# Kernel tuning notes

Hardware: AMD Instinct MI355X
Metric: run time of the kernel (lower is better)

The kernel has to match this reference:

```python
import jax, jax.numpy as jnp
import numpy as np

B, H, W, K = 4, 512, 512, 8
BKG_DEPTH = 100.0  # sentinel depth for empty pixels, as in the torch module


def setup_inputs() -> dict:
    key = jax.random.key(0)
    k1, k2, k3 = jax.random.split(key, 3)
    pixel_colors = jax.random.uniform(k1, (B, H, W, K, 4), dtype=jnp.float32)
    zbuf = jax.random.normal(k2, (B, H, W, K), dtype=jnp.float32)  # <0 => invalid fragment
    pixel_labels = jax.random.randint(k3, (B, H, W, K), 0, K, dtype=jnp.int32)
    background_color = jnp.ones((3,), jnp.float32)
    return {
        "pixel_colors": pixel_colors,
        "zbuf": zbuf,
        "pixel_labels": pixel_labels,
        "background_color": background_color,
    }


def _composite(pixel_colors, zbuf, labels_f, background_color):
    """Back-to-front alpha-over compositing scan across the K layer axis."""
    Bq, Hq, Wq, Kd, _ = pixel_colors.shape
    # layer axis to front, reversed so scan runs k = K-1 .. 0 (back to front)
    cols = jnp.moveaxis(pixel_colors, 3, 0)[::-1]  # [K,B,H,W,4]
    deps = jnp.moveaxis(zbuf, 3, 0)[::-1]          # [K,B,H,W]
    labs = jnp.moveaxis(labels_f, 3, 0)[::-1]      # [K,B,H,W]

    rgb0 = jnp.broadcast_to(background_color.astype(pixel_colors.dtype), (Bq, Hq, Wq, 3)) + 0.0
    a0 = jnp.zeros((Bq, Hq, Wq), pixel_colors.dtype)
    d0 = jnp.full((Bq, Hq, Wq), BKG_DEPTH, pixel_colors.dtype)
    l0 = jnp.full((Bq, Hq, Wq), float(Kd), pixel_colors.dtype)

    def step(carry, x):
        rgb, a, d, lab = carry
        c, z, l = x
        alpha = c[..., 3]
        rgb = c[..., :3] * alpha[..., None] + rgb * (1.0 - alpha[..., None])
        a = jnp.maximum(alpha, a)
        d = jnp.where(z > 0, z * alpha + d * (1.0 - alpha), d)
        lab = jnp.where(jnp.isfinite(l), jnp.where(alpha > 0.5, l, lab), lab)
        return (rgb, a, d, lab), None

    (rgb, a, d, lab), _ = jax.lax.scan(step, (rgb0, a0, d0, l0), (cols, deps, labs))
    img = jnp.concatenate([rgb, a[..., None]], axis=-1)  # [B,H,W,4]
    return img, d, lab


def _human_images(pixel_colors, labels_int, background_color):
    """For each label n in [0,K): gather the first (front-most) fragment with that label."""
    Bq, Hq, Wq, Kd, C = pixel_colors.shape
    N = Kd
    hit = labels_int[..., None] == jnp.arange(N, dtype=labels_int.dtype)  # [B,H,W,K,N]
    hit = jnp.concatenate([hit, jnp.ones((Bq, Hq, Wq, 1, N), bool)], axis=3)  # void layer always hits
    first = jnp.argmax(hit, axis=3)  # [B,H,W,N], first k where label matches, else K
    pcv = jnp.concatenate(
        [pixel_colors, jnp.zeros((Bq, Hq, Wq, 1, C), pixel_colors.dtype)], axis=3
    )  # [B,H,W,K+1,4]
    gathered = jnp.take_along_axis(pcv, first[..., None], axis=3)  # [B,H,W,N,4]
    alpha = gathered[..., 3:4]
    rgb = gathered[..., :3] * alpha + background_color * (1.0 - alpha)
    return jnp.concatenate([rgb, alpha], axis=-1)  # [B,H,W,N,4]


def reference(pixel_colors, zbuf, pixel_labels, background_color):
    Kd = pixel_colors.shape[3]
    # labels as float with NaN marking invalid fragments (zbuf < 0), as in torch forward
    labels_f = jnp.where(zbuf < 0, jnp.nan, pixel_labels.astype(pixel_colors.dtype))
    composite_image, composite_depth, lab = _composite(pixel_colors, zbuf, labels_f, background_color)
    # labels as ints with -1 marking invalid, as in raster_each_labeled_human
    labels_int = jnp.where(zbuf < 0, -1, pixel_labels.astype(jnp.int32))
    human_images = _human_images(pixel_colors, labels_int, background_color)
    lab = jnp.where(lab > Kd - 0.5, -1.0, lab)
    composite_label = jnp.round(lab).astype(jnp.int32)
    return composite_image, composite_depth, composite_label, human_images
```

## Files before the change

kernel.cpp:

```cpp
#include <hip/hip_runtime.h>


#define BKG_DEPTH 100.0f
#define KD 8

__global__ __launch_bounds__(256) void alpha_comp_kernel(
    const float4* __restrict__ pc,
    const float4* __restrict__ zb,
    const int4*  __restrict__ lb,
    const float* __restrict__ bg,
    float* __restrict__ out,
    int P)
{
    int pix = blockIdx.x * blockDim.x + threadIdx.x;
    if (pix >= P) return;

    const float bg0 = bg[0], bg1 = bg[1], bg2 = bg[2];

    float4 c[KD];
#pragma unroll
    for (int k = 0; k < KD; ++k) c[k] = pc[(size_t)pix * KD + k];

    float4 z0 = zb[(size_t)pix * 2 + 0];
    float4 z1 = zb[(size_t)pix * 2 + 1];
    float z[KD] = {z0.x, z0.y, z0.z, z0.w, z1.x, z1.y, z1.z, z1.w};

    int4 l0 = lb[(size_t)pix * 2 + 0];
    int4 l1 = lb[(size_t)pix * 2 + 1];
    int lbl[KD] = {l0.x, l0.y, l0.z, l0.w, l1.x, l1.y, l1.z, l1.w};

    float r = bg0, g = bg1, b = bg2;
    float a = 0.0f, d = BKG_DEPTH, lab = (float)KD;
#pragma unroll
    for (int k = KD - 1; k >= 0; --k) {
        const float alpha = c[k].w;
        const float ia = 1.0f - alpha;
        r = c[k].x * alpha + r * ia;
        g = c[k].y * alpha + g * ia;
        b = c[k].z * alpha + b * ia;
        a = fmaxf(alpha, a);
        if (z[k] > 0.0f) d = z[k] * alpha + d * ia;
        if (!(z[k] < 0.0f) && alpha > 0.5f) lab = (float)lbl[k];
    }
    const float labv = (lab > (float)KD - 0.5f) ? -1.0f : lab;

    float4 hv[KD];
#pragma unroll
    for (int n = 0; n < KD; ++n) {
        float4 gat = make_float4(0.0f, 0.0f, 0.0f, 0.0f);
#pragma unroll
        for (int k = KD - 1; k >= 0; --k) {
            if (!(z[k] < 0.0f) && lbl[k] == n) gat = c[k];
        }
        const float alpha = gat.w;
        const float ia = 1.0f - alpha;
        hv[n] = make_float4(gat.x * alpha + bg0 * ia,
                            gat.y * alpha + bg1 * ia,
                            gat.z * alpha + bg2 * ia,
                            alpha);
    }

    float4* outImg = (float4*)out;
    outImg[pix] = make_float4(r, g, b, a);
    out[(size_t)4 * P + pix] = d;
    out[(size_t)5 * P + pix] = labv;
    float4* outH = (float4*)(out + (size_t)6 * P);
#pragma unroll
    for (int n = 0; n < KD; ++n) outH[(size_t)pix * KD + n] = hv[n];
}

extern "C" void kernel_launch(void* const* d_in, const int* in_sizes, int n_in,
                              void* d_out, int out_size, void* d_ws, size_t ws_size,
                              hipStream_t stream) {
    const float4* pc = (const float4*)d_in[0];
    const float4* zb = (const float4*)d_in[1];
    const int4*  lb  = (const int4*)d_in[2];
    const float* bg  = (const float*)d_in[3];
    float* out = (float*)d_out;

    const int P = in_sizes[1] / KD;
    const int block = 256;
    const int grid = (P + block - 1) / block;
    alpha_comp_kernel<<<grid, block, 0, stream>>>(pc, zb, lb, bg, out, P);
}
```

Baseline: 308.3 us.

## Map one thread per fragment and composite with warp-shuffle scans

The per-pixel serial loop over K layers becomes eight lanes per pixel, one per fragment. The compositing recurrence is rewritten as a product scan of transmittances followed by shuffle reductions, and the label and per-human gathers use ballot and shuffles. Loads and the human-image stores become fully coalesced per lane, and each thread holds far fewer registers. In exchange there are many more shuffles, and floating-point summation order changes.

```diff
diff --git a/kernel.cpp b/kernel.cpp
--- a/kernel.cpp
+++ b/kernel.cpp
@@ -6,80 +6,111 @@
 
 __global__ __launch_bounds__(256) void alpha_comp_kernel(
     const float4* __restrict__ pc,
-    const float4* __restrict__ zb,
-    const int4*  __restrict__ lb,
-    const float* __restrict__ bg,
+    const float*  __restrict__ zb,
+    const int*    __restrict__ lb,
+    const float*  __restrict__ bg,
     float* __restrict__ out,
     int P)
 {
-    int pix = blockIdx.x * blockDim.x + threadIdx.x;
+    const int tid = blockIdx.x * blockDim.x + threadIdx.x;
+    const int pix = tid >> 3;
+    const int kk  = tid & 7;
     if (pix >= P) return;
 
     const float bg0 = bg[0], bg1 = bg[1], bg2 = bg[2];
 
-    float4 c[KD];
-#pragma unroll
-    for (int k = 0; k < KD; ++k) c[k] = pc[(size_t)pix * KD + k];
+    const float4 c   = pc[tid];
+    const float  z   = zb[tid];
+    const int    lbl = lb[tid];
+    const float  alpha = c.w;
 
-    float4 z0 = zb[(size_t)pix * 2 + 0];
-    float4 z1 = zb[(size_t)pix * 2 + 1];
-    float z[KD] = {z0.x, z0.y, z0.z, z0.w, z1.x, z1.y, z1.z, z1.w};
+    float t = 1.0f - alpha;
+    float incl = t;
+    {
+        float u;
+        u = __shfl_up(incl, 1, 8); if (kk >= 1) incl *= u;
+        u = __shfl_up(incl, 2, 8); if (kk >= 2) incl *= u;
+        u = __shfl_up(incl, 4, 8); if (kk >= 4) incl *= u;
+    }
+    float pre = __shfl_up(incl, 1, 8); if (kk == 0) pre = 1.0f;
+    const float T = __shfl(incl, 7, 8);
+    const float w = alpha * pre;
 
-    int4 l0 = lb[(size_t)pix * 2 + 0];
-    int4 l1 = lb[(size_t)pix * 2 + 1];
-    int lbl[KD] = {l0.x, l0.y, l0.z, l0.w, l1.x, l1.y, l1.z, l1.w};
+    float sr = c.x * w, sg = c.y * w, sb = c.z * w;
+    sr += __shfl_xor(sr, 1, 8); sr += __shfl_xor(sr, 2, 8); sr += __shfl_xor(sr, 4, 8);
+    sg += __shfl_xor(sg, 1, 8); sg += __shfl_xor(sg, 2, 8); sg += __shfl_xor(sg, 4, 8);
+    sb += __shfl_xor(sb, 1, 8); sb += __shfl_xor(sb, 2, 8); sb += __shfl_xor(sb, 4, 8);
+    const float outR = sr + bg0 * T;
+    const float outG = sg + bg1 * T;
+    const float outB = sb + bg2 * T;
 
-    float r = bg0, g = bg1, b = bg2;
-    float a = 0.0f, d = BKG_DEPTH, lab = (float)KD;
-#pragma unroll
-    for (int k = KD - 1; k >= 0; --k) {
-        const float alpha = c[k].w;
-        const float ia = 1.0f - alpha;
-        r = c[k].x * alpha + r * ia;
-        g = c[k].y * alpha + g * ia;
-        b = c[k].z * alpha + b * ia;
-        a = fmaxf(alpha, a);
-        if (z[k] > 0.0f) d = z[k] * alpha + d * ia;
-        if (!(z[k] < 0.0f) && alpha > 0.5f) lab = (float)lbl[k];
+    float am = alpha;
+    am = fmaxf(am, __shfl_xor(am, 1, 8));
+    am = fmaxf(am, __shfl_xor(am, 2, 8));
+    am = fmaxf(am, __shfl_xor(am, 4, 8));
+
+    const float a2 = (z > 0.0f) ? alpha : 0.0f;
+    float incl2 = 1.0f - a2;
+    {
+        float u;
+        u = __shfl_up(incl2, 1, 8); if (kk >= 1) incl2 *= u;
+        u = __shfl_up(incl2, 2, 8); if (kk >= 2) incl2 *= u;
+        u = __shfl_up(incl2, 4, 8); if (kk >= 4) incl2 *= u;
     }
-    const float labv = (lab > (float)KD - 0.5f) ? -1.0f : lab;
+    float pre2 = __shfl_up(incl2, 1, 8); if (kk == 0) pre2 = 1.0f;
+    const float T2 = __shfl(incl2, 7, 8);
+    float sd = z * (a2 * pre2);
+    sd += __shfl_xor(sd, 1, 8); sd += __shfl_xor(sd, 2, 8); sd += __shfl_xor(sd, 4, 8);
+    const float outD = sd + BKG_DEPTH * T2;
 
-    float4 hv[KD];
-#pragma unroll
-    for (int n = 0; n < KD; ++n) {
-        float4 gat = make_float4(0.0f, 0.0f, 0.0f, 0.0f);
-#pragma unroll
-        for (int k = KD - 1; k >= 0; --k) {
-            if (!(z[k] < 0.0f) && lbl[k] == n) gat = c[k];
-        }
-        const float alpha = gat.w;
-        const float ia = 1.0f - alpha;
-        hv[n] = make_float4(gat.x * alpha + bg0 * ia,
-                            gat.y * alpha + bg1 * ia,
-                            gat.z * alpha + bg2 * ia,
-                            alpha);
-    }
+    const bool validL = !(z < 0.0f);
+    const unsigned long long bal = __ballot(validL && (alpha > 0.5f));
+    const int lane = threadIdx.x & 63;
+    const unsigned int grpByte = (unsigned int)((bal >> (lane & ~7)) & 0xFFull);
+    const int jlab = grpByte ? (__ffs(grpByte) - 1) : 0;
+    const int lsel = __shfl(lbl, jlab, 8);
+    const float labv = grpByte ? (float)lsel : -1.0f;
 
-    float4* outImg = (float4*)out;
-    outImg[pix] = make_float4(r, g, b, a);
-    out[(size_t)4 * P + pix] = d;
-    out[(size_t)5 * P + pix] = labv;
-    float4* outH = (float4*)(out + (size_t)6 * P);
-#pragma unroll
-    for (int n = 0; n < KD; ++n) outH[(size_t)pix * KD + n] = hv[n];
+    const int enc = validL ? lbl : 255;
+    int jm = -1, ej;
+    ej = __shfl(enc, 7, 8); if (ej == kk) jm = 7;
+    ej = __shfl(enc, 6, 8); if (ej == kk) jm = 6;
+    ej = __shfl(enc, 5, 8); if (ej == kk) jm = 5;
+    ej = __shfl(enc, 4, 8); if (ej == kk) jm = 4;
+    ej = __shfl(enc, 3, 8); if (ej == kk) jm = 3;
+    ej = __shfl(enc, 2, 8); if (ej == kk) jm = 2;
+    ej = __shfl(enc, 1, 8); if (ej == kk) jm = 1;
+    ej = __shfl(enc, 0, 8); if (ej == kk) jm = 0;
+    const int src = (jm >= 0) ? jm : 0;
+    float gx = __shfl(c.x, src, 8);
+    float gy = __shfl(c.y, src, 8);
+    float gz = __shfl(c.z, src, 8);
+    float gw = __shfl(c.w, src, 8);
+    if (jm < 0) { gx = 0.0f; gy = 0.0f; gz = 0.0f; gw = 0.0f; }
+    const float ia = 1.0f - gw;
+    const float4 hv = make_float4(gx * gw + bg0 * ia,
+                                  gy * gw + bg1 * ia,
+                                  gz * gw + bg2 * ia,
+                                  gw);
+
+    ((float4*)(out + (size_t)6 * P))[tid] = hv;
+    if (kk == 0) ((float4*)out)[pix] = make_float4(outR, outG, outB, am);
+    if (kk == 1) out[(size_t)4 * P + pix] = outD;
+    if (kk == 2) out[(size_t)5 * P + pix] = labv;
 }
 
 extern "C" void kernel_launch(void* const* d_in, const int* in_sizes, int n_in,
                               void* d_out, int out_size, void* d_ws, size_t ws_size,
                               hipStream_t stream) {
     const float4* pc = (const float4*)d_in[0];
-    const float4* zb = (const float4*)d_in[1];
-    const int4*  lb  = (const int4*)d_in[2];
-    const float* bg  = (const float*)d_in[3];
+    const float*  zb = (const float*)d_in[1];
+    const int*    lb = (const int*)d_in[2];
+    const float*  bg = (const float*)d_in[3];
     float* out = (float*)d_out;
 
     const int P = in_sizes[1] / KD;
+    const int total = P * KD;
     const int block = 256;
-    const int grid = (P + block - 1) / block;
+    const int grid = (total + block - 1) / block;
     alpha_comp_kernel<<<grid, block, 0, stream>>>(pc, zb, lb, bg, out, P);
 }
```

Measured after the change: 292.1 us. 5.3% less time.

## Stage per-pixel fragment loads and human-image stores through padded LDS for coalescing

Applied to the files above, without the earlier changes.

Pixel colors are loaded cooperatively into shared memory with fully coalesced float4 reads, using a padded stride of 9 to avoid bank conflicts. Each thread then reads its own 8 fragments from shared memory. The per-label human-image outputs are written back the same way, through LDS, so the global stores are contiguous across threads. The bounds check is removed and the grid assumes P is a multiple of 256, and the kernel now uses 36KB of LDS per block, which may lower occupancy.

```diff
diff --git a/kernel.cpp b/kernel.cpp
--- a/kernel.cpp
+++ b/kernel.cpp
@@ -7,27 +7,38 @@
 __global__ __launch_bounds__(256) void alpha_comp_kernel(
     const float4* __restrict__ pc,
     const float4* __restrict__ zb,
-    const int4*  __restrict__ lb,
-    const float* __restrict__ bg,
+    const int4*   __restrict__ lb,
+    const float*  __restrict__ bg,
     float* __restrict__ out,
     int P)
 {
-    int pix = blockIdx.x * blockDim.x + threadIdx.x;
-    if (pix >= P) return;
+    __shared__ float4 lds[256 * 9];
+
+    const int t = threadIdx.x;
+    const int pix = blockIdx.x * 256 + t;
+    const size_t fragBase = (size_t)blockIdx.x * 2048;
 
     const float bg0 = bg[0], bg1 = bg[1], bg2 = bg[2];
 
+#pragma unroll
+    for (int i = 0; i < 8; ++i) {
+        const int f = i * 256 + t;
+        const float4 v = pc[fragBase + f];
+        lds[(f >> 3) * 9 + (f & 7)] = v;
+    }
+    __syncthreads();
+
     float4 c[KD];
 #pragma unroll
-    for (int k = 0; k < KD; ++k) c[k] = pc[(size_t)pix * KD + k];
+    for (int k = 0; k < KD; ++k) c[k] = lds[t * 9 + k];
 
-    float4 z0 = zb[(size_t)pix * 2 + 0];
-    float4 z1 = zb[(size_t)pix * 2 + 1];
-    float z[KD] = {z0.x, z0.y, z0.z, z0.w, z1.x, z1.y, z1.z, z1.w};
+    const float4 z0 = zb[(size_t)pix * 2 + 0];
+    const float4 z1 = zb[(size_t)pix * 2 + 1];
+    const float z[KD] = {z0.x, z0.y, z0.z, z0.w, z1.x, z1.y, z1.z, z1.w};
 
-    int4 l0 = lb[(size_t)pix * 2 + 0];
-    int4 l1 = lb[(size_t)pix * 2 + 1];
-    int lbl[KD] = {l0.x, l0.y, l0.z, l0.w, l1.x, l1.y, l1.z, l1.w};
+    const int4 l0 = lb[(size_t)pix * 2 + 0];
+    const int4 l1 = lb[(size_t)pix * 2 + 1];
+    const int lbl[KD] = {l0.x, l0.y, l0.z, l0.w, l1.x, l1.y, l1.z, l1.w};
 
     float r = bg0, g = bg1, b = bg2;
     float a = 0.0f, d = BKG_DEPTH, lab = (float)KD;
@@ -60,13 +71,20 @@
                             alpha);
     }
 
-    float4* outImg = (float4*)out;
-    outImg[pix] = make_float4(r, g, b, a);
+    ((float4*)out)[pix] = make_float4(r, g, b, a);
     out[(size_t)4 * P + pix] = d;
     out[(size_t)5 * P + pix] = labv;
+
+#pragma unroll
+    for (int n = 0; n < KD; ++n) lds[t * 9 + n] = hv[n];
+    __syncthreads();
+
     float4* outH = (float4*)(out + (size_t)6 * P);
 #pragma unroll
-    for (int n = 0; n < KD; ++n) outH[(size_t)pix * KD + n] = hv[n];
+    for (int i = 0; i < 8; ++i) {
+        const int f = i * 256 + t;
+        outH[fragBase + f] = lds[(f >> 3) * 9 + (f & 7)];
+    }
 }
 
 extern "C" void kernel_launch(void* const* d_in, const int* in_sizes, int n_in,
@@ -74,12 +92,12 @@
                               hipStream_t stream) {
     const float4* pc = (const float4*)d_in[0];
     const float4* zb = (const float4*)d_in[1];
-    const int4*  lb  = (const int4*)d_in[2];
-    const float* bg  = (const float*)d_in[3];
+    const int4*   lb = (const int4*)d_in[2];
+    const float*  bg = (const float*)d_in[3];
     float* out = (float*)d_out;
 
     const int P = in_sizes[1] / KD;
     const int block = 256;
-    const int grid = (P + block - 1) / block;
+    const int grid = P / block;
     alpha_comp_kernel<<<grid, block, 0, stream>>>(pc, zb, lb, bg, out, P);
 }
```

Result: no change. 303.2 us (-1.7%).
